# Performance work log

Hardware: AMD Instinct MI355X
Metric: run time of the kernel (lower is better)

Reference implementation:

```python
import jax, jax.numpy as jnp
import numpy as np

U = 512   # units
D = 512   # decoder input feature dim
V = 46    # output vocab


def _lstm_cell(x_t, h, c, W, R, b):
    # Keras LSTMCell: gate order i, f, g(cell), o; sigmoid recurrent act, tanh act.
    z = x_t @ W + h @ R + b                      # [B, 4U]
    i, f, g, o = jnp.split(z, 4, axis=-1)
    i = jax.nn.sigmoid(i)
    f = jax.nn.sigmoid(f)
    g = jnp.tanh(g)
    o = jax.nn.sigmoid(o)
    c_new = f * c + i * g
    h_new = o * jnp.tanh(c_new)
    return h_new, c_new


def _lstm_seq(seq, W, R, b):
    # seq: [T, B, D]; zero initial state (Keras default). Returns (all h [T,B,U], last h [B,U]).
    B = seq.shape[1]
    u = R.shape[0]
    h0 = jnp.zeros((B, u), seq.dtype)
    c0 = jnp.zeros((B, u), seq.dtype)
    def step(carry, x_t):
        h, c = carry
        h, c = _lstm_cell(x_t, h, c, W, R, b)
        return (h, c), h
    (hT, _), hs = jax.lax.scan(step, (h0, c0), seq)
    return hs, hT


def setup_inputs() -> dict:
    key = jax.random.key(0)
    ks = jax.random.split(key, 10)
    def p(k, shape, scale=0.05):
        return jax.random.normal(k, shape, dtype=jnp.float32) * scale
    x = jax.random.normal(ks[0], (32, 512, U), dtype=jnp.float32)   # encoder outputs [B, S, U]
    y = jax.random.normal(ks[1], (32, 128, D), dtype=jnp.float32)   # decoder inputs  [B, T, D]
    return {
        "x": x, "y": y,
        "W_a": p(ks[2], (D, 4 * U)), "R_a": p(ks[3], (U, 4 * U)), "b_a": jnp.zeros((4 * U,), jnp.float32),
        "W1": p(ks[4], (U, 4 * U)), "R1": p(ks[5], (U, 4 * U)), "b1": jnp.zeros((4 * U,), jnp.float32),
        "W2": p(ks[6], (U, 4 * U)), "R2": p(ks[7], (U, 4 * U)), "b2": jnp.zeros((4 * U,), jnp.float32),
        "Wd": p(ks[8], (U, V)), "bd": jnp.zeros((V,), jnp.float32),
    }


def reference(x, y, W_a, R_a, b_a, W1, R1, b1, W2, R2, b2, Wd, bd):
    B = y.shape[0]
    yT = jnp.swapaxes(y, 0, 1)                          # [T, B, D]
    h0 = jnp.zeros((B, U), x.dtype)
    c0 = jnp.zeros((B, U), x.dtype)

    # AttentionLSTM: per-step LSTMCell + dot-product attention (Keras Attention,
    # unscaled, keys==values==x) + residual add of the context into both states.
    def step(carry, y_t):
        h, c = carry
        h, c = _lstm_cell(y_t, h, c, W_a, R_a, b_a)     # s = h  [B, U]
        scores = jnp.einsum('bu,bsu->bs', h, x)         # [B, S]
        ctx = jnp.einsum('bs,bsu->bu', jax.nn.softmax(scores, axis=-1), x)  # [B, U]
        return (h + ctx, c + ctx), ctx

    _, ctxs = jax.lax.scan(step, (h0, c0), yT)          # [T, B, U]

    # Stacked LSTMs: first returns full sequence, second returns last hidden state.
    hs1, _ = _lstm_seq(ctxs, W1, R1, b1)                # [T, B, U]
    _, hT = _lstm_seq(hs1, W2, R2, b2)                  # [B, U]

    logits = hT @ Wd + bd                               # [B, V]
    return jax.nn.softmax(logits, axis=-1)
```

## Files before the change

kernel.cpp:

```cpp
#include <hip/hip_runtime.h>
#include <math.h>


#define U_   512
#define S_   512
#define T_   128
#define B_   32
#define G4   2048
#define V_   46
#define NWG  256
#define FSTR 32

#define AT_LD(p)     __hip_atomic_load((p), __ATOMIC_RELAXED, __HIP_MEMORY_SCOPE_AGENT)
#define AT_ST(p, v)  __hip_atomic_store((p), (v), __ATOMIC_RELAXED, __HIP_MEMORY_SCOPE_AGENT)

__device__ __forceinline__ void group_bar(unsigned* gflags, unsigned seq) {
  __syncthreads();
  const int tid = threadIdx.x;
  if (tid < 32) {
    if (tid == 0)
      AT_ST(&gflags[(blockIdx.x & 31) * FSTR], seq);
    while (!__all(AT_LD(&gflags[tid * FSTR]) >= seq))
      __builtin_amdgcn_s_sleep(1);
  }
  __syncthreads();
}

__global__ __launch_bounds__(256) void gemm_k512(
    const float* __restrict__ A, const float* __restrict__ W,
    const float* __restrict__ b, float* __restrict__ Z) {
  const int tid = threadIdx.x;
  const int j = blockIdx.x * 1024 + tid * 4;
  const int i0 = blockIdx.y * 8;
  float4 bj = *(const float4*)(b + j);
  float4 acc[8];
#pragma unroll
  for (int r = 0; r < 8; ++r) acc[r] = bj;
  const float* Arow = A + (size_t)i0 * U_;
  for (int k = 0; k < U_; ++k) {
    float4 w = *(const float4*)(W + (size_t)k * G4 + j);
#pragma unroll
    for (int r = 0; r < 8; ++r) {
      float a = Arow[(size_t)r * U_ + k];
      acc[r].x = fmaf(a, w.x, acc[r].x);
      acc[r].y = fmaf(a, w.y, acc[r].y);
      acc[r].z = fmaf(a, w.z, acc[r].z);
      acc[r].w = fmaf(a, w.w, acc[r].w);
    }
  }
#pragma unroll
  for (int r = 0; r < 8; ++r)
    *(float4*)(Z + (size_t)(i0 + r) * G4 + j) = acc[r];
}

__global__ __launch_bounds__(256) void transpose_R(
    const float* __restrict__ R, float* __restrict__ RT) {
  __shared__ float tile[64][65];
  const int c0 = blockIdx.x * 64, k0 = blockIdx.y * 64;
  const int tc = threadIdx.x & 63, tr = threadIdx.x >> 6;
  for (int r = tr; r < 64; r += 4)
    tile[r][tc] = R[(size_t)(k0 + r) * G4 + c0 + tc];
  __syncthreads();
  for (int r = tr; r < 64; r += 4)
    RT[(size_t)(c0 + r) * 512 + k0 + tc] = tile[tc][r];
}

__global__ __launch_bounds__(512) void attn_coop(
    const float* __restrict__ x, const float* __restrict__ ZY,
    const float* __restrict__ RT, float* __restrict__ ctxs,
    float* hbuf, float* hnbuf, float* smax, float* ssumg,
    float* ctxpart, unsigned* flags) {
  extern __shared__ float dyn[];
  float* x_s  = dyn;
  float* h_st = dyn + 512 * 65;
  __shared__ float zp[4][64][2];
  __shared__ float p_s[64];
  __shared__ float ctx_s[64];

  const int tid = threadIdx.x;
  const int bid = blockIdx.x;
  const int g    = bid >> 5;
  const int wgid = bid & 31;
  const int u0   = wgid * 16;
  const int kh  = tid & 1;
  const int b_l = (tid >> 1) & 3;
  const int col = tid >> 3;
  const int zcol = (col >> 4) * 512 + u0 + (col & 15);
  const int b_att = 4 * g + (wgid >> 3);
  const int sc = wgid & 7;
  unsigned* gflags = flags + g * 32 * FSTR;

  for (int idx = tid; idx < 64 * 512; idx += 512) {
    int sl = idx >> 9, u = idx & 511;
    x_s[u * 65 + sl] = x[((size_t)b_att * S_ + sc * 64 + sl) * U_ + u];
  }
  float c = 0.f, hn_reg = 0.f;
  unsigned seq = 0;
  __syncthreads();

  for (int t = 0; t < T_; ++t) {
    {
      const float4* hb4 =
          (const float4*)(hbuf + (size_t)t * 16384 + 4 * g * 512);
      float4 v = hb4[tid];
      *(float4*)(h_st + (tid >> 7) * 516 + (tid & 127) * 4) = v;
    }
    __syncthreads();
    {
      const float4* H4 = (const float4*)(h_st + b_l * 516 + kh * 256);
      const float4* R4 = (const float4*)(RT + (size_t)zcol * 512 + kh * 256);
      float acc = 0.f;
#pragma unroll 8
      for (int i = 0; i < 64; ++i) {
        float4 hv = H4[i];
        float4 rv = R4[i];
        acc = fmaf(hv.x, rv.x, acc); acc = fmaf(hv.y, rv.y, acc);
        acc = fmaf(hv.z, rv.z, acc); acc = fmaf(hv.w, rv.w, acc);
      }
      zp[b_l][col][kh] = acc;
    }
    __syncthreads();
    if (tid < 64) {
      const int bb = tid >> 4, uu = tid & 15;
      const int b = 4 * g + bb, u = u0 + uu;
      const float* zy = ZY + ((size_t)b * T_ + t) * G4 + u;
      float zi = zy[0]    + zp[bb][uu][0]      + zp[bb][uu][1];
      float zf = zy[512]  + zp[bb][16 + uu][0] + zp[bb][16 + uu][1];
      float zg = zy[1024] + zp[bb][32 + uu][0] + zp[bb][32 + uu][1];
      float zo = zy[1536] + zp[bb][48 + uu][0] + zp[bb][48 + uu][1];
      float ig = 1.f / (1.f + expf(-zi));
      float fg = 1.f / (1.f + expf(-zf));
      float gg = tanhf(zg);
      float og = 1.f / (1.f + expf(-zo));
      c = fg * c + ig * gg;
      hn_reg = og * tanhf(c);
      AT_ST(&hnbuf[(size_t)t * 16384 + b * 512 + u], hn_reg);
    }
    group_bar(gflags, ++seq);

    {
      const int wv = tid >> 6, ln = tid & 63;
      const float* hnb = hnbuf + (size_t)t * 16384 + b_att * 512;
      float hreg[8];
#pragma unroll
      for (int k = 0; k < 8; ++k) hreg[k] = hnb[ln + 64 * k];
      for (int si = 0; si < 8; ++si) {
        const int sl = wv * 8 + si;
        float a = 0.f;
#pragma unroll
        for (int k = 0; k < 8; ++k)
          a = fmaf(hreg[k], x_s[(ln + 64 * k) * 65 + sl], a);
#pragma unroll
        for (int off = 32; off; off >>= 1) a += __shfl_down(a, off);
        if (ln == 0) p_s[sl] = a;
      }
    }
    __syncthreads();
    if (tid < 64) {
      float v = p_s[tid];
      float m = v;
#pragma unroll
      for (int off = 32; off; off >>= 1) m = fmaxf(m, __shfl_down(m, off));
      m = __shfl(m, 0);
      float ex = expf(v - m);
      p_s[tid] = ex;
      float sm = ex;
#pragma unroll
      for (int off = 32; off; off >>= 1) sm += __shfl_down(sm, off);
      if (tid == 0) {
        AT_ST(&smax[b_att * 8 + sc], m);
        AT_ST(&ssumg[b_att * 8 + sc], sm);
      }
    }
    __syncthreads();
    {
      float a = 0.f;
      const float* xr = x_s + tid * 65;
#pragma unroll 8
      for (int s = 0; s < 64; ++s) a = fmaf(p_s[s], xr[s], a);
      AT_ST(&ctxpart[((size_t)b_att * 8 + sc) * 512 + tid], a);
    }
    group_bar(gflags, ++seq);

    {
      const int j = tid & 7;
      const int pair = tid >> 3;
      const int bb = pair >> 4, uu = pair & 15;
      const int b = 4 * g + bb, u = u0 + uu;
      float lm = AT_LD(&smax[b * 8 + j]);
      float ss = AT_LD(&ssumg[b * 8 + j]);
      float cp = AT_LD(&ctxpart[((size_t)b * 8 + j) * 512 + u]);
      float gm = lm;
#pragma unroll
      for (int off = 1; off < 8; off <<= 1)
        gm = fmaxf(gm, __shfl_xor(gm, off));
      float w = expf(lm - gm);
      float st = ss * w, cs = cp * w;
#pragma unroll
      for (int off = 1; off < 8; off <<= 1) {
        st += __shfl_xor(st, off);
        cs += __shfl_xor(cs, off);
      }
      if (j == 0) ctx_s[pair] = cs / st;
    }
    __syncthreads();
    if (tid < 64) {
      const int bb = tid >> 4, uu = tid & 15;
      const int b = 4 * g + bb, u = u0 + uu;
      float ctxv = ctx_s[tid];
      c += ctxv;
      float hcar = hn_reg + ctxv;
      AT_ST(&hbuf[(size_t)(t + 1) * 16384 + b * 512 + u], hcar);
      ctxs[((size_t)b * T_ + t) * U_ + u] = ctxv;
    }
    group_bar(gflags, ++seq);
  }
}

__global__ __launch_bounds__(512) void lstm_coop(
    const float* __restrict__ Zin, const float* __restrict__ R,
    float* __restrict__ seq_out, float* __restrict__ last_out,
    float* hbuf, unsigned* flags) {
  extern __shared__ float dyn[];
  float* R_s  = dyn;
  float* h_st = dyn + 64 * 516;
  __shared__ float zp[4][64][2];
  const int tid = threadIdx.x;
  const int bid = blockIdx.x;
  const int g    = bid >> 5;
  const int wgid = bid & 31;
  const int u0   = wgid * 16;
  const int kh  = tid & 1;
  const int b_l = (tid >> 1) & 3;
  const int col = tid >> 3;
  unsigned* gflags = flags + g * 32 * FSTR;

  for (int idx = tid; idx < 64 * 512; idx += 512) {
    int cc = idx & 63, kk = idx >> 6;
    R_s[cc * 516 + kk] = R[(size_t)kk * G4 + (cc >> 4) * 512 + u0 + (cc & 15)];
  }
  float c = 0.f;
  unsigned seq = 0;
  __syncthreads();

  for (int t = 0; t < T_; ++t) {
    {
      const float4* hb4 =
          (const float4*)(hbuf + (size_t)t * 16384 + 4 * g * 512);
      float4 v = hb4[tid];
      *(float4*)(h_st + (tid >> 7) * 516 + (tid & 127) * 4) = v;
    }
    __syncthreads();
    {
      const float4* H4 = (const float4*)(h_st + b_l * 516 + kh * 256);
      const float4* R4 = (const float4*)(R_s + col * 516 + kh * 256);
      float acc = 0.f;
#pragma unroll 8
      for (int i = 0; i < 64; ++i) {
        float4 hv = H4[i];
        float4 rv = R4[i];
        acc = fmaf(hv.x, rv.x, acc); acc = fmaf(hv.y, rv.y, acc);
        acc = fmaf(hv.z, rv.z, acc); acc = fmaf(hv.w, rv.w, acc);
      }
      zp[b_l][col][kh] = acc;
    }
    __syncthreads();
    if (tid < 64) {
      const int bb = tid >> 4, uu = tid & 15;
      const int b = 4 * g + bb, u = u0 + uu;
      const float* zy = Zin + ((size_t)b * T_ + t) * G4 + u;
      float zi = zy[0]    + zp[bb][uu][0]      + zp[bb][uu][1];
      float zf = zy[512]  + zp[bb][16 + uu][0] + zp[bb][16 + uu][1];
      float zg = zy[1024] + zp[bb][32 + uu][0] + zp[bb][32 + uu][1];
      float zo = zy[1536] + zp[bb][48 + uu][0] + zp[bb][48 + uu][1];
      float ig = 1.f / (1.f + expf(-zi));
      float fg = 1.f / (1.f + expf(-zf));
      float gg = tanhf(zg);
      float og = 1.f / (1.f + expf(-zo));
      c = fg * c + ig * gg;
      float hv2 = og * tanhf(c);
      AT_ST(&hbuf[(size_t)(t + 1) * 16384 + b * 512 + u], hv2);
      if (seq_out) seq_out[((size_t)b * T_ + t) * U_ + u] = hv2;
      if (last_out && t == T_ - 1) last_out[b * U_ + u] = hv2;
    }
    group_bar(gflags, ++seq);
  }
}

__global__ __launch_bounds__(64) void final_k(
    const float* __restrict__ hT, const float* __restrict__ Wd,
    const float* __restrict__ bd, float* __restrict__ out) {
  const int b = blockIdx.x;
  const int v = threadIdx.x;
  float acc = (v < V_) ? bd[v] : -INFINITY;
  if (v < V_) {
    for (int k = 0; k < U_; ++k)
      acc = fmaf(hT[(size_t)b * U_ + k], Wd[(size_t)k * V_ + v], acc);
  }
  float m = acc;
#pragma unroll
  for (int off = 32; off; off >>= 1) m = fmaxf(m, __shfl_down(m, off));
  m = __shfl(m, 0);
  float e = (v < V_) ? expf(acc - m) : 0.f;
  float s = e;
#pragma unroll
  for (int off = 32; off; off >>= 1) s += __shfl_down(s, off);
  s = __shfl(s, 0);
  if (v < V_) out[(size_t)b * V_ + v] = e / s;
}

extern "C" void kernel_launch(void* const* d_in, const int* in_sizes, int n_in,
                              void* d_out, int out_size, void* d_ws, size_t ws_size,
                              hipStream_t stream) {
  const float* x   = (const float*)d_in[0];
  const float* y   = (const float*)d_in[1];
  const float* W_a = (const float*)d_in[2];
  const float* R_a = (const float*)d_in[3];
  const float* b_a = (const float*)d_in[4];
  const float* W1  = (const float*)d_in[5];
  const float* R1  = (const float*)d_in[6];
  const float* b1  = (const float*)d_in[7];
  const float* W2  = (const float*)d_in[8];
  const float* R2  = (const float*)d_in[9];
  const float* b2  = (const float*)d_in[10];
  const float* Wd  = (const float*)d_in[11];
  const float* bd  = (const float*)d_in[12];
  float* out = (float*)d_out;

  float* ZBUF  = (float*)d_ws;
  float* SEQ   = ZBUF + (size_t)8388608;
  float* RT    = SEQ + (size_t)2097152;
  float* HROT  = RT + (size_t)1048576;
  float* HNROT = HROT + (size_t)2113536;
  float* SMAX  = HNROT + (size_t)2097152;
  float* SSUM  = SMAX + 256;
  float* CTXP  = SSUM + 256;
  float* HT    = CTXP + 131072;
  unsigned* BAR = (unsigned*)(HT + 16384);

  const int REGION = 8 * 32 * FSTR;
  unsigned* FLG_A = BAR;
  unsigned* FLG_1 = BAR + REGION;
  unsigned* FLG_2 = BAR + 2 * REGION;

  const int attn_lds = (512 * 65 + 4 * 516) * 4;
  const int lstm_lds = (64 * 516 + 4 * 516) * 4;
  hipFuncSetAttribute((const void*)attn_coop,
                      hipFuncAttributeMaxDynamicSharedMemorySize, attn_lds);
  hipFuncSetAttribute((const void*)lstm_coop,
                      hipFuncAttributeMaxDynamicSharedMemorySize, lstm_lds);

  dim3 ggrid(2, 512);
  hipMemsetAsync(BAR, 0, 3 * REGION * 4, stream);

  gemm_k512<<<ggrid, 256, 0, stream>>>(y, W_a, b_a, ZBUF);
  transpose_R<<<dim3(32, 8), 256, 0, stream>>>(R_a, RT);
  hipMemsetAsync(HROT, 0, 16384 * 4, stream);
  attn_coop<<<NWG, 512, attn_lds, stream>>>(x, ZBUF, RT, SEQ, HROT, HNROT,
                                            SMAX, SSUM, CTXP, FLG_A);
  gemm_k512<<<ggrid, 256, 0, stream>>>(SEQ, W1, b1, ZBUF);
  hipMemsetAsync(HROT, 0, 16384 * 4, stream);
  lstm_coop<<<NWG, 512, lstm_lds, stream>>>(ZBUF, R1, SEQ, nullptr, HROT,
                                            FLG_1);
  gemm_k512<<<ggrid, 256, 0, stream>>>(SEQ, W2, b2, ZBUF);
  hipMemsetAsync(HROT, 0, 16384 * 4, stream);
  lstm_coop<<<NWG, 512, lstm_lds, stream>>>(ZBUF, R2, nullptr, HT, HROT,
                                            FLG_2);
  final_k<<<B_, 64, 0, stream>>>(HT, Wd, bd, out);
}
```

Measured before the change: 3.990 ms.

## Repartition attention kernel per batch so barriers span eight workgroups

Each workgroup in the attention recurrence now owns one batch element and 64 units, in place of 4 batches × 16 units. All data dependencies then stay within the 8 workgroups of the same batch, so the grid-group barrier shrinks from 32 participants to 8. The recurrent matvec now reads 256 R rows per workgroup for a single batch, so R traffic per workgroup rises 4x while h staging shrinks. The goal is lower barrier latency on the serial 128-step chain, with more L2 traffic for R as the cost.

```diff
diff --git a/kernel.cpp b/kernel.cpp
--- a/kernel.cpp
+++ b/kernel.cpp
@@ -26,6 +26,19 @@
   __syncthreads();
 }
 
+__device__ __forceinline__ void group_bar8(unsigned* gflags, unsigned seq,
+                                           int sc) {
+  __syncthreads();
+  const int tid = threadIdx.x;
+  if (tid < 8) {
+    if (tid == 0)
+      AT_ST(&gflags[sc * FSTR], seq);
+    while (!__all(AT_LD(&gflags[tid * FSTR]) >= seq))
+      __builtin_amdgcn_s_sleep(1);
+  }
+  __syncthreads();
+}
+
 __global__ __launch_bounds__(256) void gemm_k512(
     const float* __restrict__ A, const float* __restrict__ W,
     const float* __restrict__ b, float* __restrict__ Z) {
@@ -73,41 +86,33 @@
   extern __shared__ float dyn[];
   float* x_s  = dyn;
   float* h_st = dyn + 512 * 65;
-  __shared__ float zp[4][64][2];
+  __shared__ float zp[256][2];
   __shared__ float p_s[64];
   __shared__ float ctx_s[64];
 
   const int tid = threadIdx.x;
   const int bid = blockIdx.x;
-  const int g    = bid >> 5;
-  const int wgid = bid & 31;
-  const int u0   = wgid * 16;
-  const int kh  = tid & 1;
-  const int b_l = (tid >> 1) & 3;
-  const int col = tid >> 3;
-  const int zcol = (col >> 4) * 512 + u0 + (col & 15);
-  const int b_att = 4 * g + (wgid >> 3);
-  const int sc = wgid & 7;
-  unsigned* gflags = flags + g * 32 * FSTR;
+  const int b   = bid >> 3;
+  const int sc  = bid & 7;
+  const int u0  = sc * 64;
+  const int kh   = tid & 1;
+  const int colh = tid >> 1;
+  const int zcol = (colh >> 6) * 512 + u0 + (colh & 63);
+  unsigned* gflags = flags + b * 8 * FSTR;
 
   for (int idx = tid; idx < 64 * 512; idx += 512) {
     int sl = idx >> 9, u = idx & 511;
-    x_s[u * 65 + sl] = x[((size_t)b_att * S_ + sc * 64 + sl) * U_ + u];
+    x_s[u * 65 + sl] = x[((size_t)b * S_ + u0 + sl) * U_ + u];
   }
   float c = 0.f, hn_reg = 0.f;
   unsigned seq = 0;
   __syncthreads();
 
   for (int t = 0; t < T_; ++t) {
-    {
-      const float4* hb4 =
-          (const float4*)(hbuf + (size_t)t * 16384 + 4 * g * 512);
-      float4 v = hb4[tid];
-      *(float4*)(h_st + (tid >> 7) * 516 + (tid & 127) * 4) = v;
-    }
-    __syncthreads();
-    {
-      const float4* H4 = (const float4*)(h_st + b_l * 516 + kh * 256);
+    h_st[tid] = hbuf[(size_t)t * 16384 + b * 512 + tid];
+    __syncthreads();
+    {
+      const float4* H4 = (const float4*)(h_st + kh * 256);
       const float4* R4 = (const float4*)(RT + (size_t)zcol * 512 + kh * 256);
       float acc = 0.f;
 #pragma unroll 8
@@ -117,17 +122,16 @@
         acc = fmaf(hv.x, rv.x, acc); acc = fmaf(hv.y, rv.y, acc);
         acc = fmaf(hv.z, rv.z, acc); acc = fmaf(hv.w, rv.w, acc);
       }
-      zp[b_l][col][kh] = acc;
+      zp[colh][kh] = acc;
     }
     __syncthreads();
     if (tid < 64) {
-      const int bb = tid >> 4, uu = tid & 15;
-      const int b = 4 * g + bb, u = u0 + uu;
+      const int u = u0 + tid;
       const float* zy = ZY + ((size_t)b * T_ + t) * G4 + u;
-      float zi = zy[0]    + zp[bb][uu][0]      + zp[bb][uu][1];
-      float zf = zy[512]  + zp[bb][16 + uu][0] + zp[bb][16 + uu][1];
-      float zg = zy[1024] + zp[bb][32 + uu][0] + zp[bb][32 + uu][1];
-      float zo = zy[1536] + zp[bb][48 + uu][0] + zp[bb][48 + uu][1];
+      float zi = zy[0]    + zp[tid][0]       + zp[tid][1];
+      float zf = zy[512]  + zp[64 + tid][0]  + zp[64 + tid][1];
+      float zg = zy[1024] + zp[128 + tid][0] + zp[128 + tid][1];
+      float zo = zy[1536] + zp[192 + tid][0] + zp[192 + tid][1];
       float ig = 1.f / (1.f + expf(-zi));
       float fg = 1.f / (1.f + expf(-zf));
       float gg = tanhf(zg);
@@ -136,11 +140,11 @@
       hn_reg = og * tanhf(c);
       AT_ST(&hnbuf[(size_t)t * 16384 + b * 512 + u], hn_reg);
     }
-    group_bar(gflags, ++seq);
+    group_bar8(gflags, ++seq, sc);
 
     {
       const int wv = tid >> 6, ln = tid & 63;
-      const float* hnb = hnbuf + (size_t)t * 16384 + b_att * 512;
+      const float* hnb = hnbuf + (size_t)t * 16384 + b * 512;
       float hreg[8];
 #pragma unroll
       for (int k = 0; k < 8; ++k) hreg[k] = hnb[ln + 64 * k];
@@ -168,8 +172,8 @@
 #pragma unroll
       for (int off = 32; off; off >>= 1) sm += __shfl_down(sm, off);
       if (tid == 0) {
-        AT_ST(&smax[b_att * 8 + sc], m);
-        AT_ST(&ssumg[b_att * 8 + sc], sm);
+        AT_ST(&smax[b * 8 + sc], m);
+        AT_ST(&ssumg[b * 8 + sc], sm);
       }
     }
     __syncthreads();
@@ -178,18 +182,16 @@
       const float* xr = x_s + tid * 65;
 #pragma unroll 8
       for (int s = 0; s < 64; ++s) a = fmaf(p_s[s], xr[s], a);
-      AT_ST(&ctxpart[((size_t)b_att * 8 + sc) * 512 + tid], a);
-    }
-    group_bar(gflags, ++seq);
+      AT_ST(&ctxpart[((size_t)b * 8 + sc) * 512 + tid], a);
+    }
+    group_bar8(gflags, ++seq, sc);
 
     {
       const int j = tid & 7;
-      const int pair = tid >> 3;
-      const int bb = pair >> 4, uu = pair & 15;
-      const int b = 4 * g + bb, u = u0 + uu;
+      const int uu = tid >> 3;
       float lm = AT_LD(&smax[b * 8 + j]);
       float ss = AT_LD(&ssumg[b * 8 + j]);
-      float cp = AT_LD(&ctxpart[((size_t)b * 8 + j) * 512 + u]);
+      float cp = AT_LD(&ctxpart[((size_t)b * 8 + j) * 512 + u0 + uu]);
       float gm = lm;
 #pragma unroll
       for (int off = 1; off < 8; off <<= 1)
@@ -201,19 +203,18 @@
         st += __shfl_xor(st, off);
         cs += __shfl_xor(cs, off);
       }
-      if (j == 0) ctx_s[pair] = cs / st;
+      if (j == 0) ctx_s[uu] = cs / st;
     }
     __syncthreads();
     if (tid < 64) {
-      const int bb = tid >> 4, uu = tid & 15;
-      const int b = 4 * g + bb, u = u0 + uu;
+      const int u = u0 + tid;
       float ctxv = ctx_s[tid];
       c += ctxv;
       float hcar = hn_reg + ctxv;
       AT_ST(&hbuf[(size_t)(t + 1) * 16384 + b * 512 + u], hcar);
       ctxs[((size_t)b * T_ + t) * U_ + u] = ctxv;
     }
-    group_bar(gflags, ++seq);
+    group_bar8(gflags, ++seq, sc);
   }
 }
 
@@ -338,12 +339,12 @@
   float* HT    = CTXP + 131072;
   unsigned* BAR = (unsigned*)(HT + 16384);
 
-  const int REGION = 8 * 32 * FSTR;
+  const int REGION = 8192;
   unsigned* FLG_A = BAR;
   unsigned* FLG_1 = BAR + REGION;
   unsigned* FLG_2 = BAR + 2 * REGION;
 
-  const int attn_lds = (512 * 65 + 4 * 516) * 4;
+  const int attn_lds = (512 * 65 + 512) * 4;
   const int lstm_lds = (64 * 516 + 4 * 516) * 4;
   hipFuncSetAttribute((const void*)attn_coop,
                       hipFuncAttributeMaxDynamicSharedMemorySize, attn_lds);
```

New measurement: 4.884 ms. 1.22x slower.
